# Kernel tuning notes

Measured on AMD Instinct MI355X. Metric: run time of the kernel, lower is better.

The kernel has to match this reference:

```python
import jax, jax.numpy as jnp
import numpy as np

EMBED_DIM = 1024
NUM_HEADS = 16
DIM_HEAD = EMBED_DIM // NUM_HEADS


def setup_inputs() -> dict:
    key = jax.random.key(0)
    ks = jax.random.split(key, 9)
    s = 1.0 / np.sqrt(EMBED_DIM)
    x = jax.random.normal(ks[0], (2, 2048, EMBED_DIM), dtype=jnp.float32)
    Wq = jax.random.uniform(ks[1], (EMBED_DIM, EMBED_DIM), jnp.float32, -s, s)
    bq = jax.random.uniform(ks[2], (EMBED_DIM,), jnp.float32, -s, s)
    Wk = jax.random.uniform(ks[3], (EMBED_DIM, EMBED_DIM), jnp.float32, -s, s)
    bk = jax.random.uniform(ks[4], (EMBED_DIM,), jnp.float32, -s, s)
    Wv = jax.random.uniform(ks[5], (EMBED_DIM, EMBED_DIM), jnp.float32, -s, s)
    bv = jax.random.uniform(ks[6], (EMBED_DIM,), jnp.float32, -s, s)
    Wo = jax.random.uniform(ks[7], (EMBED_DIM, EMBED_DIM), jnp.float32, -s, s)
    bo = jax.random.uniform(ks[8], (EMBED_DIM,), jnp.float32, -s, s)
    return {"x": x, "Wq": Wq, "bq": bq, "Wk": Wk, "bk": bk,
            "Wv": Wv, "bv": bv, "Wo": Wo, "bo": bo}


def reference(x, Wq, bq, Wk, bk, Wv, bv, Wo, bo):
    B, S, _ = x.shape
    # Linear layers (torch nn.Linear: x @ W.T + b), reshape to heads
    Q = (x @ Wq.T + bq).reshape(B, S, NUM_HEADS, DIM_HEAD)
    K = (x @ Wk.T + bk).reshape(B, S, NUM_HEADS, DIM_HEAD)
    V = (x @ Wv.T + bv).reshape(B, S, NUM_HEADS, DIM_HEAD)
    scores = jnp.einsum('bqhd,bkhd->bhqk', Q, K) / np.sqrt(DIM_HEAD)
    attn = jax.nn.softmax(scores, axis=-1)
    context = jnp.einsum('bhqk,bkhd->bqhd', attn, V).reshape(B, S, EMBED_DIM)
    return context @ Wo.T + bo
```

## Files before the change

### kernel.cpp

```cpp
#include <hip/hip_runtime.h>
#include <hip/hip_bf16.h>

#define SEQ   2048
#define EMB   1024
#define NHEAD 16
#define DHEAD 64
#define BATCH 2
#define MTOT  (BATCH*SEQ)
#define QT    128
#define KT    64

typedef __attribute__((ext_vector_type(8))) short s8v;
typedef __attribute__((ext_vector_type(4))) short s4v;
typedef __attribute__((ext_vector_type(4))) float f4v;

__device__ __forceinline__ short f2b(float f) {
    union { float fl; unsigned u; } v; v.fl = f;
    unsigned u = v.u;
    u = (u + 0x7fffu + ((u >> 16) & 1u)) >> 16;
    return (short)u;
}
__device__ __forceinline__ unsigned pk2(float a, float b) {
    union { __hip_bfloat162 h; unsigned u; } c;
    c.h = __float22bfloat162_rn(float2{a, b});
    return c.u;
}

#if __has_builtin(__builtin_amdgcn_exp2f)
__device__ __forceinline__ float exp2_fast(float x) { return __builtin_amdgcn_exp2f(x); }
#else
__device__ __forceinline__ float exp2_fast(float x) { return exp2f(x); }
#endif

__device__ __forceinline__ void bar_lds() {
    asm volatile("s_waitcnt lgkmcnt(0)\n\ts_barrier" ::: "memory");
}

__device__ __forceinline__ void gl_lds16(const short* g, short* l) {
    __builtin_amdgcn_global_load_lds(
        (const __attribute__((address_space(1))) void*)g,
        (__attribute__((address_space(3))) void*)l, 16, 0, 0);
}

__global__ __launch_bounds__(256)
void cvt_swz(const float* __restrict__ s0, const float* __restrict__ s1,
             const float* __restrict__ s2, const float* __restrict__ s3,
             const float* __restrict__ s4,
             short* __restrict__ d0, short* __restrict__ d1,
             short* __restrict__ d2, short* __restrict__ d3,
             short* __restrict__ d4)
{
    const int seg = blockIdx.y;
    const float* s = seg == 0 ? s0 : seg == 1 ? s1 : seg == 2 ? s2 : seg == 3 ? s3 : s4;
    short*       d = seg == 0 ? d0 : seg == 1 ? d1 : seg == 2 ? d2 : seg == 3 ? d3 : d4;
    const int nchunk = (seg == 0 ? MTOT * EMB : EMB * EMB) / 8;
    const int stride = gridDim.x * 256;
    for (int i = blockIdx.x * 256 + threadIdx.x; i < nchunk; i += stride) {
        const int row = i >> 7;
        const int c   = i & 127;
        const float4 v0 = *(const float4*)(s + (size_t)i * 8);
        const float4 v1 = *(const float4*)(s + (size_t)i * 8 + 4);
        s8v o;
        o[0] = f2b(v0.x); o[1] = f2b(v0.y); o[2] = f2b(v0.z); o[3] = f2b(v0.w);
        o[4] = f2b(v1.x); o[5] = f2b(v1.y); o[6] = f2b(v1.z); o[7] = f2b(v1.w);
        const int cp = (c & ~7) | ((c & 7) ^ (row & 7));
        *(s8v*)(d + (size_t)row * EMB + cp * 8) = o;
    }
}

template<int NT, bool FUSED3>
__global__ __launch_bounds__(256, 3)
void gemm_bb3(const short* __restrict__ A,
              const short* __restrict__ W0, const short* __restrict__ W1, const short* __restrict__ W2,
              const float* __restrict__ B0, const float* __restrict__ B1, const float* __restrict__ B2,
              void* __restrict__ C0, void* __restrict__ C1, void* __restrict__ C2)
{
    constexpr int JN = NT / 32;
    const int K = EMB, N = EMB;
    const int ntiles = EMB / NT;
    const int mat = blockIdx.x / ntiles;
    const int n0  = (blockIdx.x % ntiles) * NT;
    const int m0  = blockIdx.y * 128;
    const short* W  = (mat == 0) ? W0 : (mat == 1 ? W1 : W2);
    const float* Bi = (mat == 0) ? B0 : (mat == 1 ? B1 : B2);
    void*        C  = (mat == 0) ? C0 : (mat == 1 ? C1 : C2);
    const float qscale = (FUSED3 && mat == 0) ? 0.18033688f : 1.0f;

    __shared__ __align__(16) short As[128 * 64];
    __shared__ __align__(16) short Ws[NT * 64];

    const int tid  = threadIdx.x;
    const int lane = tid & 63;
    const int wave = tid >> 6;
    const int quad = lane >> 4;
    const int l16  = lane & 15;
    const int l8   = l16 & 7;
    const int wm   = wave >> 1;
    const int wn   = wave & 1;

    f4v acc[4][JN] = {};

    const int srow = lane >> 3;
    const int scol = (lane & 7) * 8;

    for (int k0 = 0; k0 < K; k0 += 64) {
        #pragma unroll
        for (int p = 0; p < 4; ++p) {
            const int rbase = wave * 32 + p * 8;
            gl_lds16(A + (size_t)(m0 + rbase + srow) * K + k0 + scol,
                     As + rbase * 64);
        }
        #pragma unroll
        for (int p = 0; p < NT / 32; ++p) {
            const int rbase = wave * (NT / 4) + p * 8;
            gl_lds16(W + (size_t)(n0 + rbase + srow) * K + k0 + scol,
                     Ws + rbase * 64);
        }
        __syncthreads();

        #pragma unroll
        for (int kk = 0; kk < 2; ++kk) {
            const int slot = ((kk * 4 + quad) ^ l8) * 8;
            s8v af[4], wf[JN];
            #pragma unroll
            for (int i = 0; i < 4; ++i)
                af[i] = *(const s8v*)(As + (wm * 64 + i * 16 + l16) * 64 + slot);
            #pragma unroll
            for (int j = 0; j < JN; ++j)
                wf[j] = *(const s8v*)(Ws + (wn * (NT / 2) + j * 16 + l16) * 64 + slot);
            #pragma unroll
            for (int i = 0; i < 4; ++i)
                #pragma unroll
                for (int j = 0; j < JN; ++j)
                    acc[i][j] = __builtin_amdgcn_mfma_f32_16x16x32_bf16(
                        af[i], wf[j], acc[i][j], 0, 0, 0);
        }
        __syncthreads();
    }

    #pragma unroll
    for (int j = 0; j < JN; ++j) {
        const int n = n0 + wn * (NT / 2) + j * 16 + l16;
        const float bv = Bi[n];
        #pragma unroll
        for (int i = 0; i < 4; ++i) {
            const int mb = m0 + wm * 64 + i * 16 + quad * 4;
            if (FUSED3 && mat == 2) {
                const int bb = mb >> 11, s = mb & 2047;
                s4v ov;
                #pragma unroll
                for (int rr = 0; rr < 4; ++rr) ov[rr] = f2b(acc[i][j][rr] + bv);
                *(s4v*)((short*)C + ((size_t)(bb * 1024 + n)) * SEQ + s) = ov;
            } else if (FUSED3) {
                #pragma unroll
                for (int rr = 0; rr < 4; ++rr)
                    ((short*)C)[(size_t)(mb + rr) * N + n] = f2b((acc[i][j][rr] + bv) * qscale);
            } else {
                #pragma unroll
                for (int rr = 0; rr < 4; ++rr)
                    ((float*)C)[(size_t)(mb + rr) * N + n] = acc[i][j][rr] + bv;
            }
        }
    }
}

__global__ __launch_bounds__(256, 2)
void attn_mfma4(const short* Q, const short* __restrict__ Kg,
                const short* __restrict__ Vt, short* O)
{
    const int blk = blockIdx.x;
    const int qb = blk & 15;
    const int h  = (blk >> 4) & 15;
    const int b  = blk >> 8;
    const int q0 = qb * QT;

    const int tid  = threadIdx.x;
    const int lane = tid & 63;
    const int wave = tid >> 6;
    const int quad = lane >> 4;
    const int l16  = lane & 15;
    const int l8   = l16 & 7;

    __shared__ __align__(16) short Ks[2][64 * 64];
    __shared__ __align__(16) short Vs[2][64 * 64];
    __shared__ __align__(16) short Pt[QT * 64];

    s8v qf[2][2];
    #pragma unroll
    for (int mi = 0; mi < 2; ++mi)
        #pragma unroll
        for (int kk = 0; kk < 2; ++kk)
            qf[mi][kk] = *(const s8v*)(Q + (size_t)(b * SEQ + q0 + wave * 32 + mi * 16 + l16) * EMB
                                         + h * DHEAD + kk * 32 + quad * 8);

    f4v oacc[4][2] = {};
    f4v sacc[2]    = {};
    s8v onef;
    #pragma unroll
    for (int i = 0; i < 8; ++i) onef[i] = (short)0x3F80;

    const int c = tid & 7, r = tid >> 3;
    const int swz = (c ^ (r & 7)) * 8;
    const size_t kbase = (size_t)(b * SEQ) * EMB + h * DHEAD;
    const size_t vbase = (size_t)((b * NHEAD + h) * DHEAD) * SEQ;

    s8v ka[2], va[2];
    #pragma unroll
    for (int p = 0; p < 2; ++p) {
        ka[p] = *(const s8v*)(Kg + kbase + (size_t)(r + p * 32) * EMB + c * 8);
        va[p] = *(const s8v*)(Vt + vbase + (size_t)(r + p * 32) * SEQ + c * 8);
    }

    for (int t = 0; t < SEQ / KT; ++t) {
        const int buf = t & 1;
        short* KsB = Ks[buf];
        short* VsB = Vs[buf];

        #pragma unroll
        for (int p = 0; p < 2; ++p) {
            *(s8v*)(KsB + (r + p * 32) * 64 + swz) = ka[p];
            *(s8v*)(VsB + (r + p * 32) * 64 + swz) = va[p];
        }
        if (t + 1 < SEQ / KT) {
            const int kt2 = (t + 1) * KT;
            #pragma unroll
            for (int p = 0; p < 2; ++p) {
                ka[p] = *(const s8v*)(Kg + kbase + (size_t)(kt2 + r + p * 32) * EMB + c * 8);
                va[p] = *(const s8v*)(Vt + vbase + (size_t)(r + p * 32) * SEQ + kt2 + c * 8);
            }
        }
        bar_lds();

        f4v sc[4][2] = {};
        #pragma unroll
        for (int kk = 0; kk < 2; ++kk) {
            const int ko = ((kk * 4 + quad) ^ l8) * 8;
            s8v kf[4];
            #pragma unroll
            for (int j = 0; j < 4; ++j)
                kf[j] = *(const s8v*)(KsB + (j * 16 + l16) * 64 + ko);
            #pragma unroll
            for (int j = 0; j < 4; ++j)
                #pragma unroll
                for (int mi = 0; mi < 2; ++mi)
                    sc[j][mi] = __builtin_amdgcn_mfma_f32_16x16x32_bf16(
                        kf[j], qf[mi][kk], sc[j][mi], 0, 0, 0);
        }

        #pragma unroll
        for (int j = 0; j < 4; ++j)
            #pragma unroll
            for (int mi = 0; mi < 2; ++mi) {
                union { unsigned u[2]; s4v s; } pv;
                pv.u[0] = pk2(exp2_fast(sc[j][mi][0]), exp2_fast(sc[j][mi][1]));
                pv.u[1] = pk2(exp2_fast(sc[j][mi][2]), exp2_fast(sc[j][mi][3]));
                const int pc = ((j * 2 + (quad >> 1)) ^ l8) * 8 + (quad & 1) * 4;
                *(s4v*)(Pt + (wave * 32 + mi * 16 + l16) * 64 + pc) = pv.s;
            }

        #pragma unroll
        for (int kk = 0; kk < 2; ++kk) {
            const int ko = ((kk * 4 + quad) ^ l8) * 8;
            s8v pf[2];
            #pragma unroll
            for (int mi = 0; mi < 2; ++mi) {
                pf[mi] = *(const s8v*)(Pt + (wave * 32 + mi * 16 + l16) * 64 + ko);
                sacc[mi] = __builtin_amdgcn_mfma_f32_16x16x32_bf16(
                    onef, pf[mi], sacc[mi], 0, 0, 0);
            }
            #pragma unroll
            for (int j = 0; j < 4; ++j) {
                const s8v vf = *(const s8v*)(VsB + (j * 16 + l16) * 64 + ko);
                #pragma unroll
                for (int mi = 0; mi < 2; ++mi)
                    oacc[j][mi] = __builtin_amdgcn_mfma_f32_16x16x32_bf16(
                        vf, pf[mi], oacc[j][mi], 0, 0, 0);
            }
        }
    }

    float inv[2];
    #pragma unroll
    for (int mi = 0; mi < 2; ++mi) inv[mi] = 1.0f / sacc[mi][0];

    #pragma unroll
    for (int j = 0; j < 4; ++j)
        #pragma unroll
        for (int mi = 0; mi < 2; ++mi) {
            union { unsigned u[2]; s4v s; } ov;
            ov.u[0] = pk2(oacc[j][mi][0] * inv[mi], oacc[j][mi][1] * inv[mi]);
            ov.u[1] = pk2(oacc[j][mi][2] * inv[mi], oacc[j][mi][3] * inv[mi]);
            const int pc = ((j * 2 + (quad >> 1)) ^ l8) * 8 + (quad & 1) * 4;
            *(s4v*)(Pt + (wave * 32 + mi * 16 + l16) * 64 + pc) = ov.s;
        }

    const int row = tid >> 1;
    const int cb  = (tid & 1) * 4;
    #pragma unroll
    for (int c4 = 0; c4 < 4; ++c4) {
        const int pcc = cb + c4;
        const s8v tt = *(const s8v*)(Pt + row * 64 + pcc * 8);
        *(s8v*)(O + (size_t)(b * SEQ + q0 + row) * EMB + h * DHEAD + pcc * 8) = tt;
    }
}

extern "C" void kernel_launch(void* const* d_in, const int* in_sizes, int n_in,
                              void* d_out, int out_size, void* d_ws, size_t ws_size,
                              hipStream_t stream)
{
    const float* x  = (const float*)d_in[0];
    const float* Wq = (const float*)d_in[1];
    const float* bq = (const float*)d_in[2];
    const float* Wk = (const float*)d_in[3];
    const float* bk = (const float*)d_in[4];
    const float* Wv = (const float*)d_in[5];
    const float* bv = (const float*)d_in[6];
    const float* Wo = (const float*)d_in[7];
    const float* bo = (const float*)d_in[8];
    float* out = (float*)d_out;

    short* xb  = (short*)d_ws;
    short* Wqb = xb  + (size_t)MTOT * EMB;
    short* Wkb = Wqb + (size_t)EMB * EMB;
    short* Wvb = Wkb + (size_t)EMB * EMB;
    short* Wob = Wvb + (size_t)EMB * EMB;
    short* Qw  = Wob + (size_t)EMB * EMB;
    short* Kw  = Qw  + (size_t)MTOT * EMB;
    short* Vtw = Kw  + (size_t)MTOT * EMB;

    cvt_swz<<<dim3(512, 5), 256, 0, stream>>>(x, Wq, Wk, Wv, Wo,
                                              xb, Wqb, Wkb, Wvb, Wob);

    gemm_bb3<128, true><<<dim3(24, 32), 256, 0, stream>>>(
        xb, Wqb, Wkb, Wvb, bq, bk, bv, Qw, Kw, Vtw);

    attn_mfma4<<<dim3(BATCH * NHEAD * (SEQ / QT)), 256, 0, stream>>>(Qw, Kw, Vtw, Qw);

    gemm_bb3<64, false><<<dim3(16, 32), 256, 0, stream>>>(
        Qw, Wob, Wob, Wob, bo, bo, bo, out, out, out);
}
```

Before: 182.9 us.

## Keep attention P in registers via permlane swaps, halve query tile, remap blocks to XCDs

```diff
diff --git a/kernel.cpp b/kernel.cpp
--- a/kernel.cpp
+++ b/kernel.cpp
@@ -7,7 +7,7 @@
 #define DHEAD 64
 #define BATCH 2
 #define MTOT  (BATCH*SEQ)
-#define QT    128
+#define QT    64
 #define KT    64
 
 typedef __attribute__((ext_vector_type(8))) short s8v;
@@ -31,6 +31,13 @@
 #else
 __device__ __forceinline__ float exp2_fast(float x) { return exp2f(x); }
 #endif
+
+__device__ __forceinline__ void pl32swap(unsigned &a, unsigned &b) {
+    asm("v_permlane32_swap_b32 %0, %1" : "+v"(a), "+v"(b));
+}
+__device__ __forceinline__ void pl16swap(unsigned &a, unsigned &b) {
+    asm("v_permlane16_swap_b32 %0, %1" : "+v"(a), "+v"(b));
+}
 
 __device__ __forceinline__ void bar_lds() {
     asm volatile("s_waitcnt lgkmcnt(0)\n\ts_barrier" ::: "memory");
@@ -164,14 +171,17 @@
     }
 }
 
-__global__ __launch_bounds__(256, 2)
-void attn_mfma4(const short* Q, const short* __restrict__ Kg,
+__global__ __launch_bounds__(256, 4)
+void attn_mfma6(const short* Q, const short* __restrict__ Kg,
                 const short* __restrict__ Vt, short* O)
 {
-    const int blk = blockIdx.x;
-    const int qb = blk & 15;
-    const int h  = (blk >> 4) & 15;
-    const int b  = blk >> 8;
+    const int i    = blockIdx.x;
+    const int xcd  = i & 7;
+    const int slot = i >> 3;
+    const int combo = xcd * 4 + (slot >> 5);
+    const int qb = slot & 31;
+    const int h  = combo & 15;
+    const int b  = combo >> 4;
     const int q0 = qb * QT;
 
     const int tid  = threadIdx.x;
@@ -183,21 +193,18 @@
 
     __shared__ __align__(16) short Ks[2][64 * 64];
     __shared__ __align__(16) short Vs[2][64 * 64];
-    __shared__ __align__(16) short Pt[QT * 64];
-
-    s8v qf[2][2];
-    #pragma unroll
-    for (int mi = 0; mi < 2; ++mi)
-        #pragma unroll
-        for (int kk = 0; kk < 2; ++kk)
-            qf[mi][kk] = *(const s8v*)(Q + (size_t)(b * SEQ + q0 + wave * 32 + mi * 16 + l16) * EMB
-                                         + h * DHEAD + kk * 32 + quad * 8);
-
-    f4v oacc[4][2] = {};
-    f4v sacc[2]    = {};
+
+    s8v qf[2];
+    #pragma unroll
+    for (int kk = 0; kk < 2; ++kk)
+        qf[kk] = *(const s8v*)(Q + (size_t)(b * SEQ + q0 + wave * 16 + l16) * EMB
+                                 + h * DHEAD + kk * 32 + quad * 8);
+
+    f4v oacc[4] = {};
+    f4v sacc    = {};
     s8v onef;
     #pragma unroll
-    for (int i = 0; i < 8; ++i) onef[i] = (short)0x3F80;
+    for (int e = 0; e < 8; ++e) onef[e] = (short)0x3F80;
 
     const int c = tid & 7, r = tid >> 3;
     const int swz = (c ^ (r & 7)) * 8;
@@ -231,7 +238,7 @@
         }
         bar_lds();
 
-        f4v sc[4][2] = {};
+        f4v sc[4] = {};
         #pragma unroll
         for (int kk = 0; kk < 2; ++kk) {
             const int ko = ((kk * 4 + quad) ^ l8) * 8;
@@ -241,65 +248,61 @@
                 kf[j] = *(const s8v*)(KsB + (j * 16 + l16) * 64 + ko);
             #pragma unroll
             for (int j = 0; j < 4; ++j)
-                #pragma unroll
-                for (int mi = 0; mi < 2; ++mi)
-                    sc[j][mi] = __builtin_amdgcn_mfma_f32_16x16x32_bf16(
-                        kf[j], qf[mi][kk], sc[j][mi], 0, 0, 0);
-        }
-
-        #pragma unroll
-        for (int j = 0; j < 4; ++j)
-            #pragma unroll
-            for (int mi = 0; mi < 2; ++mi) {
-                union { unsigned u[2]; s4v s; } pv;
-                pv.u[0] = pk2(exp2_fast(sc[j][mi][0]), exp2_fast(sc[j][mi][1]));
-                pv.u[1] = pk2(exp2_fast(sc[j][mi][2]), exp2_fast(sc[j][mi][3]));
-                const int pc = ((j * 2 + (quad >> 1)) ^ l8) * 8 + (quad & 1) * 4;
-                *(s4v*)(Pt + (wave * 32 + mi * 16 + l16) * 64 + pc) = pv.s;
-            }
+                sc[j] = __builtin_amdgcn_mfma_f32_16x16x32_bf16(
+                    kf[j], qf[kk], sc[j], 0, 0, 0);
+        }
+
+        unsigned u[4][2];
+        #pragma unroll
+        for (int j = 0; j < 4; ++j) {
+            u[j][0] = pk2(exp2_fast(sc[j][0]), exp2_fast(sc[j][1]));
+            u[j][1] = pk2(exp2_fast(sc[j][2]), exp2_fast(sc[j][3]));
+        }
+
+        #pragma unroll
+        for (int r2 = 0; r2 < 2; ++r2) {
+            pl32swap(u[0][r2], u[1][r2]);
+            pl32swap(u[2][r2], u[3][r2]);
+            pl16swap(u[0][r2], u[1][r2]);
+            pl16swap(u[2][r2], u[3][r2]);
+        }
+        union { unsigned uu[4]; s8v s; } pfa, pfb;
+        pfa.uu[0] = u[0][0]; pfa.uu[1] = u[0][1]; pfa.uu[2] = u[1][0]; pfa.uu[3] = u[1][1];
+        pfb.uu[0] = u[2][0]; pfb.uu[1] = u[2][1]; pfb.uu[2] = u[3][0]; pfb.uu[3] = u[3][1];
 
         #pragma unroll
         for (int kk = 0; kk < 2; ++kk) {
+            const s8v pf = kk ? pfb.s : pfa.s;
+            sacc = __builtin_amdgcn_mfma_f32_16x16x32_bf16(onef, pf, sacc, 0, 0, 0);
             const int ko = ((kk * 4 + quad) ^ l8) * 8;
-            s8v pf[2];
-            #pragma unroll
-            for (int mi = 0; mi < 2; ++mi) {
-                pf[mi] = *(const s8v*)(Pt + (wave * 32 + mi * 16 + l16) * 64 + ko);
-                sacc[mi] = __builtin_amdgcn_mfma_f32_16x16x32_bf16(
-                    onef, pf[mi], sacc[mi], 0, 0, 0);
-            }
             #pragma unroll
             for (int j = 0; j < 4; ++j) {
                 const s8v vf = *(const s8v*)(VsB + (j * 16 + l16) * 64 + ko);
-                #pragma unroll
-                for (int mi = 0; mi < 2; ++mi)
-                    oacc[j][mi] = __builtin_amdgcn_mfma_f32_16x16x32_bf16(
-                        vf, pf[mi], oacc[j][mi], 0, 0, 0);
+                oacc[j] = __builtin_amdgcn_mfma_f32_16x16x32_bf16(
+                    vf, pf, oacc[j], 0, 0, 0);
             }
         }
     }
 
-    float inv[2];
-    #pragma unroll
-    for (int mi = 0; mi < 2; ++mi) inv[mi] = 1.0f / sacc[mi][0];
-
-    #pragma unroll
-    for (int j = 0; j < 4; ++j)
-        #pragma unroll
-        for (int mi = 0; mi < 2; ++mi) {
-            union { unsigned u[2]; s4v s; } ov;
-            ov.u[0] = pk2(oacc[j][mi][0] * inv[mi], oacc[j][mi][1] * inv[mi]);
-            ov.u[1] = pk2(oacc[j][mi][2] * inv[mi], oacc[j][mi][3] * inv[mi]);
-            const int pc = ((j * 2 + (quad >> 1)) ^ l8) * 8 + (quad & 1) * 4;
-            *(s4v*)(Pt + (wave * 32 + mi * 16 + l16) * 64 + pc) = ov.s;
-        }
-
-    const int row = tid >> 1;
-    const int cb  = (tid & 1) * 4;
-    #pragma unroll
-    for (int c4 = 0; c4 < 4; ++c4) {
+    const float inv = 1.0f / sacc[0];
+
+    short* Os = (short*)Ks;
+    #pragma unroll
+    for (int j = 0; j < 4; ++j) {
+        union { unsigned uu[2]; s4v s; } ov;
+        ov.uu[0] = pk2(oacc[j][0] * inv, oacc[j][1] * inv);
+        ov.uu[1] = pk2(oacc[j][2] * inv, oacc[j][3] * inv);
+        const int pc = ((j * 2 + (quad >> 1)) ^ l8) * 8 + (quad & 1) * 4;
+        *(s4v*)(Os + (wave * 16 + l16) * 64 + pc) = ov.s;
+    }
+    bar_lds();
+
+    const int row = tid >> 2;
+    const int cb  = (tid & 3) * 2;
+    #pragma unroll
+    for (int c4 = 0; c4 < 2; ++c4) {
         const int pcc = cb + c4;
-        const s8v tt = *(const s8v*)(Pt + row * 64 + pcc * 8);
+        const s8v tt = *(const s8v*)(Os + row * 64 + pcc * 8);
         *(s8v*)(O + (size_t)(b * SEQ + q0 + row) * EMB + h * DHEAD + pcc * 8) = tt;
     }
 }
@@ -334,7 +337,7 @@
     gemm_bb3<128, true><<<dim3(24, 32), 256, 0, stream>>>(
         xb, Wqb, Wkb, Wvb, bq, bk, bv, Qw, Kw, Vtw);
 
-    attn_mfma4<<<dim3(BATCH * NHEAD * (SEQ / QT)), 256, 0, stream>>>(Qw, Kw, Vtw, Qw);
+    attn_mfma6<<<dim3(BATCH * NHEAD * (SEQ / QT)), 256, 0, stream>>>(Qw, Kw, Vtw, Qw);
 
     gemm_bb3<64, false><<<dim3(16, 32), 256, 0, stream>>>(
         Qw, Wob, Wob, Wob, bo, bo, bo, out, out, out);
```

After: 193.9 us. 6.0% more time.
